# Kernel tuning notes

Measured on AMD Instinct MI355X. Metric: run time of the kernel, lower is better.

Reference implementation:

```python
import jax, jax.numpy as jnp
import numpy as np

D_MODEL = 768
N_HEADS = 12
D_K = 768
D_V = 768
SEQ = 2048
BATCH = 2


def setup_inputs() -> dict:
    key = jax.random.key(0)
    ks = jax.random.split(key, 9)
    s = 0.02
    return {
        "x": jax.random.normal(ks[0], (SEQ, BATCH, D_MODEL), dtype=jnp.float32),
        "Wq": jax.random.normal(ks[1], (D_MODEL, D_K), dtype=jnp.float32) * s,
        "bq": jnp.zeros((D_K,), dtype=jnp.float32),
        "Wk": jax.random.normal(ks[2], (D_MODEL, D_K), dtype=jnp.float32) * s,
        "bk": jnp.zeros((D_K,), dtype=jnp.float32),
        "Wv": jax.random.normal(ks[3], (D_MODEL, D_V), dtype=jnp.float32) * s,
        "bv": jnp.zeros((D_V,), dtype=jnp.float32),
        "Wo": jax.random.normal(ks[4], (D_V, D_MODEL), dtype=jnp.float32) * s,
        "bo": jnp.zeros((D_MODEL,), dtype=jnp.float32),
    }


def reference(x, Wq, bq, Wk, bk, Wv, bv, Wo, bo):
    # x: (S, B, D)
    S, B, D = x.shape
    H = N_HEADS
    hk = D_K // H
    hv = D_V // H
    q = (x @ Wq + bq).reshape(S, B, H, hk)
    k = (x @ Wk + bk).reshape(S, B, H, hk)
    v = (x @ Wv + bv).reshape(S, B, H, hv)
    scale = 1.0 / np.sqrt(hk).astype(np.float32)
    # scores: (B, H, S_q, S_k)
    att = jnp.einsum("sbhd,tbhd->bhst", q, k) * scale
    causal = jnp.triu(jnp.ones((S, S), dtype=bool), k=1)  # True above diagonal
    att = jnp.where(causal, jnp.float32(-jnp.inf), att)
    att = jax.nn.softmax(att, axis=-1)
    y = jnp.einsum("bhst,tbhd->sbhd", att, v).reshape(S, B, D_V)
    return y @ Wo + bo  # (S, B, D)
```

## Files before the change

kernel.cpp:

```cpp
#include <hip/hip_runtime.h>

typedef __attribute__((ext_vector_type(8))) short short8;
typedef __attribute__((ext_vector_type(4))) short s16x4;
typedef __attribute__((ext_vector_type(4))) float f32x4;

#define NHEADS 12
#define SEQLEN 2048
#define HEADD  64
#define DMODEL 768

__device__ __forceinline__ short cvtbf(float f) {
  unsigned u = __builtin_bit_cast(unsigned, f);
  u += 0x7fffu + ((u >> 16) & 1u);
  return (short)(u >> 16);
}

__device__ __forceinline__ void gload16(const void* g, void* l) {
  __builtin_amdgcn_global_load_lds((const __attribute__((address_space(1))) void*)g,
                                   (__attribute__((address_space(3))) void*)l, 16, 0, 0);
}

__device__ __forceinline__ void ds_write_hi16(short* p, float v) {
  asm volatile("ds_write_b16_d16_hi %0, %1"
               : : "v"((__attribute__((address_space(3))) short*)p), "v"(v) : "memory");
}

__global__ void prep_kernel(const float* __restrict__ x, short* __restrict__ xb,
                            const float* __restrict__ w0, const float* __restrict__ w1,
                            const float* __restrict__ w2, const float* __restrict__ w3,
                            short* __restrict__ wt, short* __restrict__ wot) {
  __shared__ float t[32][33];
  const int tid = threadIdx.x;
  if (blockIdx.x < 1536) {
    int i = blockIdx.x * 256 + tid;
    const float* p = x + (size_t)i * 8;
    short8 v;
#pragma unroll
    for (int j = 0; j < 8; ++j) v[j] = cvtbf(p[j]);
    *(short8*)(xb + (size_t)i * 8) = v;
    return;
  }
  int bx = blockIdx.x - 1536;
  int bz = bx / 576, rem = bx - bz * 576;
  int bxx = rem % 24, byy = rem / 24;
  const float* W = bz == 0 ? w0 : bz == 1 ? w1 : bz == 2 ? w2 : w3;
  short* O = bz < 3 ? wt + (size_t)bz * (768 * 768) : wot;
  int tx = tid & 31, ty = tid >> 5;
  int n0 = bxx * 32, k0 = byy * 32;
#pragma unroll
  for (int j = 0; j < 4; ++j)
    t[ty + j * 8][tx] = W[(k0 + ty + j * 8) * 768 + n0 + tx];
  __syncthreads();
#pragma unroll
  for (int j = 0; j < 4; ++j)
    O[(n0 + ty + j * 8) * 768 + k0 + tx] = cvtbf(t[tx][ty + j * 8]);
}

template <bool DBUF>
__device__ __forceinline__ void gemm_core128(const short* __restrict__ A,
                                             const short* __restrict__ Bt,
                                             short* sA, short* sB,
                                             int bm, int bn, f32x4 acc[4][4]) {
  const int tid = threadIdx.x;
  const int w = tid >> 6, lane = tid & 63;
  const int quad = lane >> 4, l16 = lane & 15;
  const int wm = (w & 1) * 64, wn = (w >> 1) * 64;

  int gA[4], gB[4], lbase[4];
#pragma unroll
  for (int j = 0; j < 4; ++j) {
    int slot = j * 256 + w * 64 + lane;
    int r = slot >> 3, c = (slot & 7) ^ (r & 7);
    gA[j] = (bm * 128 + r) * 768 + c * 8;
    gB[j] = (bn * 128 + r) * 768 + c * 8;
    lbase[j] = (j * 256 + w * 64) * 8;
  }

  if (DBUF) {
#pragma unroll
    for (int j = 0; j < 4; ++j) {
      gload16(A + gA[j], sA + lbase[j]);
      gload16(Bt + gB[j], sB + lbase[j]);
    }
    int pb = 0;
    for (int kt = 0; kt < 12; ++kt) {
      __syncthreads();
      if (kt + 1 < 12) {
        int o = (pb ^ 1) * 8192;
#pragma unroll
        for (int j = 0; j < 4; ++j) {
          gload16(A + gA[j] + (kt + 1) * 64, sA + o + lbase[j]);
          gload16(Bt + gB[j] + (kt + 1) * 64, sB + o + lbase[j]);
        }
      }
      const short* pa = sA + pb * 8192;
      const short* pbv = sB + pb * 8192;
#pragma unroll
      for (int ks = 0; ks < 2; ++ks) {
        int cp = (ks * 4 + quad) ^ (l16 & 7);
        short8 a[4], b[4];
#pragma unroll
        for (int mt = 0; mt < 4; ++mt)
          a[mt] = *(const short8*)(pa + (wm + mt * 16 + l16) * 64 + cp * 8);
#pragma unroll
        for (int nt = 0; nt < 4; ++nt)
          b[nt] = *(const short8*)(pbv + (wn + nt * 16 + l16) * 64 + cp * 8);
#pragma unroll
        for (int mt = 0; mt < 4; ++mt)
#pragma unroll
          for (int nt = 0; nt < 4; ++nt)
            acc[mt][nt] = __builtin_amdgcn_mfma_f32_16x16x32_bf16(a[mt], b[nt], acc[mt][nt], 0, 0, 0);
      }
      pb ^= 1;
    }
  } else {
    for (int kt = 0; kt < 12; ++kt) {
      __syncthreads();
#pragma unroll
      for (int j = 0; j < 4; ++j) {
        gload16(A + gA[j] + kt * 64, sA + lbase[j]);
        gload16(Bt + gB[j] + kt * 64, sB + lbase[j]);
      }
      __syncthreads();
#pragma unroll
      for (int ks = 0; ks < 2; ++ks) {
        int cp = (ks * 4 + quad) ^ (l16 & 7);
        short8 a[4], b[4];
#pragma unroll
        for (int mt = 0; mt < 4; ++mt)
          a[mt] = *(const short8*)(sA + (wm + mt * 16 + l16) * 64 + cp * 8);
#pragma unroll
        for (int nt = 0; nt < 4; ++nt)
          b[nt] = *(const short8*)(sB + (wn + nt * 16 + l16) * 64 + cp * 8);
#pragma unroll
        for (int mt = 0; mt < 4; ++mt)
#pragma unroll
          for (int nt = 0; nt < 4; ++nt)
            acc[mt][nt] = __builtin_amdgcn_mfma_f32_16x16x32_bf16(a[mt], b[nt], acc[mt][nt], 0, 0, 0);
      }
    }
  }
}

__global__ __launch_bounds__(256, 3) void qkv_gemm(
    const short* __restrict__ A, const short* __restrict__ Bt,
    const float* __restrict__ bq, const float* __restrict__ bk, const float* __restrict__ bv,
    short* __restrict__ oq, short* __restrict__ ok, short* __restrict__ ov) {
  __shared__ short sA[128 * 64];
  __shared__ short sB[128 * 64];
  f32x4 acc[4][4];
  const f32x4 z4 = {0.f, 0.f, 0.f, 0.f};
#pragma unroll
  for (int mt = 0; mt < 4; ++mt)
#pragma unroll
    for (int nt = 0; nt < 4; ++nt) acc[mt][nt] = z4;

  const int bm = blockIdx.x, bn = blockIdx.y;
  gemm_core128<false>(A, Bt, sA, sB, bm, bn, acc);

  const int seg = bn / 6, bn_l = bn % 6;
  const float* bias = seg == 0 ? bq : seg == 1 ? bk : bv;
  short* outp = seg == 0 ? oq : seg == 1 ? ok : ov;

  const int tid = threadIdx.x;
  const int w = tid >> 6, lane = tid & 63;
  const int quad = lane >> 4, l16 = lane & 15;
  const int wm = (w & 1) * 64, wn = (w >> 1) * 64;

#pragma unroll
  for (int nt = 0; nt < 4; ++nt) {
    int n = bn_l * 128 + wn + nt * 16 + l16;
    float bval = bias[n];
    int h = n >> 6, d = n & 63;
#pragma unroll
    for (int mt = 0; mt < 4; ++mt) {
      int rowb = wm + mt * 16 + quad * 4;
#pragma unroll
      for (int r = 0; r < 4; ++r) {
        int m = bm * 128 + rowb + r;
        int s = m >> 1, b = m & 1;
        float v = acc[mt][nt][r] + bval;
        if (seg == 0) v *= 0.1803368801f;
        if (seg < 2)
          outp[((b * NHEADS + h) * SEQLEN + s) * HEADD + d] = cvtbf(v);
        else
          outp[((b * NHEADS + h) * HEADD + d) * SEQLEN + s] = cvtbf(v);
      }
    }
  }
}

#define AE(qi, ts, nt) ((qi) | ((ts) << 8) | ((nt) << 16))
__device__ const int ATTN_TAB[80] = {
  AE(31,0,8), AE(31,8,8), AE(31,16,8), AE(31,24,8),
  AE(30,0,8), AE(30,8,8), AE(30,16,8),
  AE(29,0,8), AE(29,8,8), AE(29,16,8),
  AE(28,0,8), AE(28,8,8), AE(28,16,8),
  AE(27,0,8), AE(27,8,8), AE(27,16,8),
  AE(26,0,8), AE(26,8,8), AE(26,16,8),
  AE(25,0,8), AE(25,8,8), AE(25,16,8),
  AE(24,0,8), AE(24,8,8), AE(24,16,8),
  AE(23,0,8), AE(23,8,8), AE(23,16,8),
  AE(22,0,8), AE(22,8,8),
  AE(21,0,8), AE(21,8,8),
  AE(20,0,8), AE(20,8,8),
  AE(19,0,8), AE(19,8,8),
  AE(18,0,8), AE(18,8,8),
  AE(17,0,8), AE(17,8,8),
  AE(16,0,8), AE(16,8,8),
  AE(15,0,8), AE(15,8,8),
  AE(14,0,8), AE(13,0,8), AE(12,0,8), AE(11,0,8),
  AE(10,0,8), AE(9,0,8),  AE(8,0,8),  AE(7,0,8),
  AE(30,24,7), AE(22,16,7), AE(14,8,7), AE(6,0,7),
  AE(29,24,6), AE(21,16,6), AE(13,8,6), AE(5,0,6),
  AE(28,24,5), AE(20,16,5), AE(12,8,5), AE(4,0,5),
  AE(27,24,4), AE(19,16,4), AE(11,8,4), AE(3,0,4),
  AE(26,24,3), AE(18,16,3), AE(10,8,3), AE(2,0,3),
  AE(25,24,2), AE(17,16,2), AE(9,8,2),  AE(1,0,2),
  AE(24,24,1), AE(16,16,1), AE(8,8,1),  AE(0,0,1),
};
__device__ const int PBASE[32] = {
  0,0,0,0,0,0,0,0,
  0,2,4,6,8,10,12,14,
  16,19,22,25,28,31,34,37,
  40,44,48,52,56,60,64,68};

__global__ __launch_bounds__(256, 4) void attn_kernel(
    const short* __restrict__ Q, const short* __restrict__ K,
    const short* __restrict__ Vt, short* __restrict__ Y,
    float* __restrict__ Of, float* __restrict__ lf) {
  __shared__ short sK[2][64 * 64];
  __shared__ short sV[2][64 * 64];
  __shared__ short sP[64 * 64];
  const int tid = threadIdx.x;
  const int w = tid >> 6, lane = tid & 63;
  const int quad = lane >> 4, l16 = lane & 15;
  const int e = ATTN_TAB[blockIdx.x / 24];
  const int bh = blockIdx.x % 24;
  const int qi = e & 255, ts = (e >> 8) & 255, ntl = e >> 16;
  const int q0 = qi << 6;
  const short* Qb = Q + (size_t)bh * (SEQLEN * HEADD);
  const short* Kb = K + (size_t)bh * (SEQLEN * HEADD);
  const short* Vb = Vt + (size_t)bh * (SEQLEN * HEADD);

  short8 aq[2];
#pragma unroll
  for (int ks = 0; ks < 2; ++ks)
    aq[ks] = *(const short8*)(Qb + (q0 + w * 16 + l16) * 64 + ks * 32 + quad * 8);

  const short8 bones = {0x3F80, 0x3F80, 0x3F80, 0x3F80, 0x3F80, 0x3F80, 0x3F80, 0x3F80};
  f32x4 acc_o[4], acc_l;
  const f32x4 z4 = {0.f, 0.f, 0.f, 0.f};
#pragma unroll
  for (int nt = 0; nt < 4; ++nt) acc_o[nt] = z4;
  acc_l = z4;

  int gK[2], gV[2], lbase[2];
#pragma unroll
  for (int j = 0; j < 2; ++j) {
    int slot = j * 256 + w * 64 + lane;
    int r = slot >> 3, c = (slot & 7) ^ (r & 7);
    gK[j] = r * 64 + c * 8;
    gV[j] = r * 2048 + c * 8;
    lbase[j] = (j * 256 + w * 64) * 8;
  }

  const int qrow = q0 + w * 16 + quad * 4;
  const int tend = ts + ntl;

#pragma unroll
  for (int j = 0; j < 2; ++j) {
    gload16(Kb + (ts << 6) * 64 + gK[j], &sK[0][lbase[j]]);
    gload16(Vb + (ts << 6) + gV[j], &sV[0][lbase[j]]);
  }

  int pb = 0;
  for (int it = ts; it < tend; ++it) {
    __syncthreads();
    if (it + 1 < tend) {
      const int t1 = (it + 1) << 6;
#pragma unroll
      for (int j = 0; j < 2; ++j) {
        gload16(Kb + t1 * 64 + gK[j], &sK[pb ^ 1][lbase[j]]);
        gload16(Vb + t1 + gV[j], &sV[pb ^ 1][lbase[j]]);
      }
    }
    const short* sk = sK[pb];
    const short* sv = sV[pb];

    f32x4 sc[4];
#pragma unroll
    for (int nt = 0; nt < 4; ++nt) sc[nt] = z4;
#pragma unroll
    for (int ks = 0; ks < 2; ++ks) {
      int cp = (ks * 4 + quad) ^ (l16 & 7);
#pragma unroll
      for (int nt = 0; nt < 4; ++nt) {
        short8 bk = *(const short8*)(sk + (nt * 16 + l16) * 64 + cp * 8);
        sc[nt] = __builtin_amdgcn_mfma_f32_16x16x32_bf16(aq[ks], bk, sc[nt], 0, 0, 0);
      }
    }

    if (it == qi) {
      const int t0 = it << 6;
#pragma unroll
      for (int nt = 0; nt < 4; ++nt)
#pragma unroll
        for (int r = 0; r < 4; ++r) {
          int t = t0 + nt * 16 + l16;
          if (t > qrow + r) sc[nt][r] = -1e30f;
        }
    }

#pragma unroll
    for (int nt = 0; nt < 4; ++nt)
#pragma unroll
      for (int r = 0; r < 4; ++r) {
        float p = __builtin_amdgcn_exp2f(sc[nt][r]);
        int rq = w * 16 + quad * 4 + r;
        int t = nt * 16 + l16;
        int c = t >> 3;
        ds_write_hi16(&sP[rq * 64 + ((c ^ (rq & 7)) * 8 + (t & 7))], p);
      }

#pragma unroll
    for (int kst = 0; kst < 2; ++kst) {
      int rq = w * 16 + l16;
      int cpa = (kst * 4 + quad) ^ (rq & 7);
      short8 ap = *(const short8*)(sP + rq * 64 + cpa * 8);
      acc_l = __builtin_amdgcn_mfma_f32_16x16x32_bf16(ap, bones, acc_l, 0, 0, 0);
#pragma unroll
      for (int nt = 0; nt < 4; ++nt) {
        int row = nt * 16 + l16;
        int cv = (kst * 4 + quad) ^ (row & 7);
        short8 bv = *(const short8*)(sv + row * 64 + cv * 8);
        acc_o[nt] = __builtin_amdgcn_mfma_f32_16x16x32_bf16(ap, bv, acc_o[nt], 0, 0, 0);
      }
    }
    pb ^= 1;
  }

  if (qi < 8) {
    const int b = bh / NHEADS, h = bh % NHEADS;
#pragma unroll
    for (int r = 0; r < 4; ++r) {
      float rl = __builtin_amdgcn_rcpf(acc_l[r]);
      int srow = q0 + w * 16 + quad * 4 + r;
#pragma unroll
      for (int nt = 0; nt < 4; ++nt)
        Y[(srow * 2 + b) * DMODEL + h * 64 + nt * 16 + l16] = cvtbf(acc_o[nt][r] * rl);
    }
  } else {
    const int slot = bh * 72 + PBASE[qi] + (ts >> 3);
    float* Ob = Of + (size_t)slot * 4096;
#pragma unroll
    for (int r = 0; r < 4; ++r) {
      int row = w * 16 + quad * 4 + r;
#pragma unroll
      for (int nt = 0; nt < 4; ++nt)
        Ob[row * 64 + nt * 16 + l16] = acc_o[nt][r];
      if (l16 == 0) lf[slot * 64 + row] = acc_l[r];
    }
  }
}

__global__ void attn_merge(const float* __restrict__ Of, const float* __restrict__ lf,
                           short* __restrict__ Y) {
  const int bh = blockIdx.x % 24, qi = 8 + blockIdx.x / 24;
  const int nch = (qi >> 3) + 1;
  const int base = bh * 72 + PBASE[qi];
  const float* O0 = Of + (size_t)base * 4096;
  const float* L0 = lf + base * 64;
  const int b = bh / NHEADS, h = bh % NHEADS;
  const int tid = threadIdx.x;
#pragma unroll
  for (int j = 0; j < 4; ++j) {
    int i4 = j * 256 + tid;
    int row = i4 >> 4, col4 = (i4 & 15) * 4;
    f32x4 o = *(const f32x4*)(O0 + (size_t)i4 * 4);
    float l = L0[row];
    for (int c = 1; c < nch; ++c) {
      o += *(const f32x4*)(O0 + (size_t)c * 4096 + (size_t)i4 * 4);
      l += L0[c * 64 + row];
    }
    float rl = __builtin_amdgcn_rcpf(l);
    s16x4 y;
#pragma unroll
    for (int k = 0; k < 4; ++k) y[k] = cvtbf(o[k] * rl);
    int srow = qi * 64 + row;
    *(s16x4*)(Y + (size_t)(srow * 2 + b) * DMODEL + h * 64 + col4) = y;
  }
}

__global__ __launch_bounds__(256, 2) void oproj_gemm(
    const short* __restrict__ A, const short* __restrict__ Bt,
    const float* __restrict__ bo, float* __restrict__ out) {
  __shared__ short sA[2 * 128 * 64];
  __shared__ short sB[2 * 128 * 64];
  f32x4 acc[4][4];
  const f32x4 z4 = {0.f, 0.f, 0.f, 0.f};
#pragma unroll
  for (int mt = 0; mt < 4; ++mt)
#pragma unroll
    for (int nt = 0; nt < 4; ++nt) acc[mt][nt] = z4;

  const int bm = blockIdx.x, bn = blockIdx.y;
  gemm_core128<true>(A, Bt, sA, sB, bm, bn, acc);

  const int tid = threadIdx.x;
  const int w = tid >> 6, lane = tid & 63;
  const int quad = lane >> 4, l16 = lane & 15;
  const int wm = (w & 1) * 64, wn = (w >> 1) * 64;

#pragma unroll
  for (int nt = 0; nt < 4; ++nt) {
    int n = bn * 128 + wn + nt * 16 + l16;
    float bval = bo[n];
#pragma unroll
    for (int mt = 0; mt < 4; ++mt) {
      int rowb = wm + mt * 16 + quad * 4;
#pragma unroll
      for (int r = 0; r < 4; ++r) {
        int m = bm * 128 + rowb + r;
        out[(size_t)m * 768 + n] = acc[mt][nt][r] + bval;
      }
    }
  }
}

extern "C" void kernel_launch(void* const* d_in, const int* in_sizes, int n_in,
                              void* d_out, int out_size, void* d_ws, size_t ws_size,
                              hipStream_t stream) {
  const float* x  = (const float*)d_in[0];
  const float* Wq = (const float*)d_in[1];
  const float* bq = (const float*)d_in[2];
  const float* Wk = (const float*)d_in[3];
  const float* bk = (const float*)d_in[4];
  const float* Wv = (const float*)d_in[5];
  const float* bv = (const float*)d_in[6];
  const float* Wo = (const float*)d_in[7];
  const float* bo = (const float*)d_in[8];
  float* out = (float*)d_out;

  short* ws  = (short*)d_ws;
  short* xb  = ws;
  short* wt  = ws + 3145728;
  short* wot = ws + 4915200;
  short* qw  = ws + 5505024;
  short* kw  = ws + 8650752;
  short* vw  = ws + 11796480;
  short* yw  = ws + 14942208;
  float* Of  = (float*)(ws + 18087936);
  float* lf  = Of + 7077888;

  prep_kernel<<<3840, 256, 0, stream>>>(x, xb, Wq, Wk, Wv, Wo, wt, wot);
  qkv_gemm<<<dim3(32, 18), 256, 0, stream>>>(xb, wt, bq, bk, bv, qw, kw, vw);
  attn_kernel<<<1920, 256, 0, stream>>>(qw, kw, vw, yw, Of, lf);
  attn_merge<<<576, 256, 0, stream>>>(Of, lf, yw);
  oproj_gemm<<<dim3(32, 6), 256, 0, stream>>>(yw, wot, bo, out);
}
```

Baseline: 153.4 us.

## Remap block indices per XCD for L2 locality and double-buffer QKV GEMM

Switches the QKV projection GEMM to the double-buffered LDS pipeline already used by the output projection, and lowers its occupancy target from 3 to 2 blocks per CU to fit the doubled shared memory. All three GEMM/attention kernels now launch as 1D grids with an index remap that places blocks sharing the same A/B tiles or the same batch-head on the same XCD, so those blocks reuse that XCD's L2. This trades some occupancy in the QKV GEMM for overlapping loads with compute and fewer cross-XCD refetches.

```diff
diff --git a/kernel.cpp b/kernel.cpp
--- a/kernel.cpp
+++ b/kernel.cpp
@@ -56,7 +56,6 @@
     O[(n0 + ty + j * 8) * 768 + k0 + tx] = cvtbf(t[tx][ty + j * 8]);
 }
 
-template <bool DBUF>
 __device__ __forceinline__ void gemm_core128(const short* __restrict__ A,
                                              const short* __restrict__ Bt,
                                              short* sA, short* sB,
@@ -76,78 +75,50 @@
     lbase[j] = (j * 256 + w * 64) * 8;
   }
 
-  if (DBUF) {
-#pragma unroll
-    for (int j = 0; j < 4; ++j) {
-      gload16(A + gA[j], sA + lbase[j]);
-      gload16(Bt + gB[j], sB + lbase[j]);
-    }
-    int pb = 0;
-    for (int kt = 0; kt < 12; ++kt) {
-      __syncthreads();
-      if (kt + 1 < 12) {
-        int o = (pb ^ 1) * 8192;
-#pragma unroll
-        for (int j = 0; j < 4; ++j) {
-          gload16(A + gA[j] + (kt + 1) * 64, sA + o + lbase[j]);
-          gload16(Bt + gB[j] + (kt + 1) * 64, sB + o + lbase[j]);
-        }
-      }
-      const short* pa = sA + pb * 8192;
-      const short* pbv = sB + pb * 8192;
-#pragma unroll
-      for (int ks = 0; ks < 2; ++ks) {
-        int cp = (ks * 4 + quad) ^ (l16 & 7);
-        short8 a[4], b[4];
-#pragma unroll
-        for (int mt = 0; mt < 4; ++mt)
-          a[mt] = *(const short8*)(pa + (wm + mt * 16 + l16) * 64 + cp * 8);
+#pragma unroll
+  for (int j = 0; j < 4; ++j) {
+    gload16(A + gA[j], sA + lbase[j]);
+    gload16(Bt + gB[j], sB + lbase[j]);
+  }
+  int pb = 0;
+  for (int kt = 0; kt < 12; ++kt) {
+    __syncthreads();
+    if (kt + 1 < 12) {
+      int o = (pb ^ 1) * 8192;
+#pragma unroll
+      for (int j = 0; j < 4; ++j) {
+        gload16(A + gA[j] + (kt + 1) * 64, sA + o + lbase[j]);
+        gload16(Bt + gB[j] + (kt + 1) * 64, sB + o + lbase[j]);
+      }
+    }
+    const short* pa = sA + pb * 8192;
+    const short* pbv = sB + pb * 8192;
+#pragma unroll
+    for (int ks = 0; ks < 2; ++ks) {
+      int cp = (ks * 4 + quad) ^ (l16 & 7);
+      short8 a[4], b[4];
+#pragma unroll
+      for (int mt = 0; mt < 4; ++mt)
+        a[mt] = *(const short8*)(pa + (wm + mt * 16 + l16) * 64 + cp * 8);
+#pragma unroll
+      for (int nt = 0; nt < 4; ++nt)
+        b[nt] = *(const short8*)(pbv + (wn + nt * 16 + l16) * 64 + cp * 8);
+#pragma unroll
+      for (int mt = 0; mt < 4; ++mt)
 #pragma unroll
         for (int nt = 0; nt < 4; ++nt)
-          b[nt] = *(const short8*)(pbv + (wn + nt * 16 + l16) * 64 + cp * 8);
-#pragma unroll
-        for (int mt = 0; mt < 4; ++mt)
-#pragma unroll
-          for (int nt = 0; nt < 4; ++nt)
-            acc[mt][nt] = __builtin_amdgcn_mfma_f32_16x16x32_bf16(a[mt], b[nt], acc[mt][nt], 0, 0, 0);
-      }
-      pb ^= 1;
-    }
-  } else {
-    for (int kt = 0; kt < 12; ++kt) {
-      __syncthreads();
-#pragma unroll
-      for (int j = 0; j < 4; ++j) {
-        gload16(A + gA[j] + kt * 64, sA + lbase[j]);
-        gload16(Bt + gB[j] + kt * 64, sB + lbase[j]);
-      }
-      __syncthreads();
-#pragma unroll
-      for (int ks = 0; ks < 2; ++ks) {
-        int cp = (ks * 4 + quad) ^ (l16 & 7);
-        short8 a[4], b[4];
-#pragma unroll
-        for (int mt = 0; mt < 4; ++mt)
-          a[mt] = *(const short8*)(sA + (wm + mt * 16 + l16) * 64 + cp * 8);
-#pragma unroll
-        for (int nt = 0; nt < 4; ++nt)
-          b[nt] = *(const short8*)(sB + (wn + nt * 16 + l16) * 64 + cp * 8);
-#pragma unroll
-        for (int mt = 0; mt < 4; ++mt)
-#pragma unroll
-          for (int nt = 0; nt < 4; ++nt)
-            acc[mt][nt] = __builtin_amdgcn_mfma_f32_16x16x32_bf16(a[mt], b[nt], acc[mt][nt], 0, 0, 0);
-      }
-    }
-  }
-}
-
-__global__ __launch_bounds__(256, 3) void qkv_gemm(
+          acc[mt][nt] = __builtin_amdgcn_mfma_f32_16x16x32_bf16(a[mt], b[nt], acc[mt][nt], 0, 0, 0);
+    }
+    pb ^= 1;
+  }
+}
+
+__global__ __launch_bounds__(256, 2) void qkv_gemm(
     const short* __restrict__ A, const short* __restrict__ Bt,
     const float* __restrict__ bq, const float* __restrict__ bk, const float* __restrict__ bv,
     short* __restrict__ oq, short* __restrict__ ok, short* __restrict__ ov) {
-  __shared__ short sA[128 * 64];
-  __shared__ short sB[128 * 64];
+  __shared__ short sA[2 * 128 * 64];
+  __shared__ short sB[2 * 128 * 64];
   f32x4 acc[4][4];
   const f32x4 z4 = {0.f, 0.f, 0.f, 0.f};
 #pragma unroll
@@ -155,8 +126,12 @@
 #pragma unroll
     for (int nt = 0; nt < 4; ++nt) acc[mt][nt] = z4;
 
-  const int bm = blockIdx.x, bn = blockIdx.y;
-  gemm_core128<false>(A, Bt, sA, sB, bm, bn, acc);
+  const int id = blockIdx.x;
+  const int xcd = id & 7, t = id >> 3;
+  const int bm = (xcd & 3) * 8 + (t & 7);
+  const int bn = (xcd >> 2) * 9 + (t >> 3);
+
+  gemm_core128(A, Bt, sA, sB, bm, bn, acc);
 
   const int seg = bn / 6, bn_l = bn % 6;
   const float* bias = seg == 0 ? bq : seg == 1 ? bk : bv;
@@ -235,8 +210,10 @@
   const int tid = threadIdx.x;
   const int w = tid >> 6, lane = tid & 63;
   const int quad = lane >> 4, l16 = lane & 15;
-  const int e = ATTN_TAB[blockIdx.x / 24];
-  const int bh = blockIdx.x % 24;
+  const int id = blockIdx.x;
+  const int xcd = id & 7, t = id >> 3;
+  const int bh = xcd * 3 + t % 3;
+  const int e = ATTN_TAB[t / 3];
   const int qi = e & 255, ts = (e >> 8) & 255, ntl = e >> 16;
   const int q0 = qi << 6;
   const short* Qb = Q + (size_t)bh * (SEQLEN * HEADD);
@@ -307,8 +284,8 @@
       for (int nt = 0; nt < 4; ++nt)
 #pragma unroll
         for (int r = 0; r < 4; ++r) {
-          int t = t0 + nt * 16 + l16;
-          if (t > qrow + r) sc[nt][r] = -1e30f;
+          int tt = t0 + nt * 16 + l16;
+          if (tt > qrow + r) sc[nt][r] = -1e30f;
         }
     }
 
@@ -318,9 +295,9 @@
       for (int r = 0; r < 4; ++r) {
         float p = __builtin_amdgcn_exp2f(sc[nt][r]);
         int rq = w * 16 + quad * 4 + r;
-        int t = nt * 16 + l16;
-        int c = t >> 3;
-        ds_write_hi16(&sP[rq * 64 + ((c ^ (rq & 7)) * 8 + (t & 7))], p);
+        int tc = nt * 16 + l16;
+        int c = tc >> 3;
+        ds_write_hi16(&sP[rq * 64 + ((c ^ (rq & 7)) * 8 + (tc & 7))], p);
       }
 
 #pragma unroll
@@ -404,8 +381,12 @@
 #pragma unroll
     for (int nt = 0; nt < 4; ++nt) acc[mt][nt] = z4;
 
-  const int bm = blockIdx.x, bn = blockIdx.y;
-  gemm_core128<true>(A, Bt, sA, sB, bm, bn, acc);
+  const int id = blockIdx.x;
+  const int xcd = id & 7, t = id >> 3;
+  const int bm = (xcd & 3) * 8 + (t & 7);
+  const int bn = (xcd >> 2) * 3 + (t >> 3);
+
+  gemm_core128(A, Bt, sA, sB, bm, bn, acc);
 
   const int tid = threadIdx.x;
   const int w = tid >> 6, lane = tid & 63;
@@ -454,8 +435,8 @@
   float* lf  = Of + 7077888;
 
   prep_kernel<<<3840, 256, 0, stream>>>(x, xb, Wq, Wk, Wv, Wo, wt, wot);
-  qkv_gemm<<<dim3(32, 18), 256, 0, stream>>>(xb, wt, bq, bk, bv, qw, kw, vw);
+  qkv_gemm<<<576, 256, 0, stream>>>(xb, wt, bq, bk, bv, qw, kw, vw);
   attn_kernel<<<1920, 256, 0, stream>>>(qw, kw, vw, yw, Of, lf);
   attn_merge<<<576, 256, 0, stream>>>(Of, lf, yw);
-  oproj_gemm<<<dim3(32, 6), 256, 0, stream>>>(yw, wot, bo, out);
-}
+  oproj_gemm<<<192, 256, 0, stream>>>(yw, wot, bo, out);
+}
```

Result: slower. 178.2 us (+16.1%).
